# Kernel optimization log

Hardware: AMD Instinct MI355X
Metric: run time of the kernel (lower is better)

## Reference

```python
import jax, jax.numpy as jnp
import numpy as np

N_HEAD = 16

def _proj(W, b, x):
    # 1x1 Conv2d: x is (b, e, h, w) -> (b, o, h, w)
    return jnp.einsum('oe,behw->bohw', W, x) + b[None, :, None, None]

def setup_inputs() -> dict:
    key = jax.random.key(0)
    ks = jax.random.split(key, 12)
    B, E, S = 2, 1024, 2048
    d_qk, d_v, d_out = E, E, E
    def xavier(k, o, i):
        bound = np.sqrt(6.0 / (o + i))
        return jax.random.uniform(k, (o, i), jnp.float32, -bound, bound)
    return {
        'q': jax.random.normal(ks[0], (B, E, 1, S), jnp.float32),
        'k': jax.random.normal(ks[1], (B, E, 1, S), jnp.float32),
        'v': jax.random.normal(ks[2], (B, E, 1, S), jnp.float32),
        'qk_mask': jax.random.normal(ks[3], (B, S, 1, S), jnp.float32),
        'Wq': xavier(ks[4], d_qk, E), 'bq': jnp.zeros((d_qk,), jnp.float32),
        'Wk': xavier(ks[5], d_qk, E), 'bk': jnp.zeros((d_qk,), jnp.float32),
        'Wv': xavier(ks[6], d_v, E), 'bv': jnp.zeros((d_v,), jnp.float32),
        'Wo': xavier(ks[7], d_out, d_v), 'bo': jnp.zeros((d_out,), jnp.float32),
    }

def reference(q, k, v, qk_mask, Wq, bq, Wk, bk, Wv, bv, Wo, bo):
    # q,k,v: (B, E, 1, S); qk_mask: (B, S_src, 1, S_tgt)
    qp = _proj(Wq, bq, q)
    kp = _proj(Wk, bk, k)
    vp = _proj(Wv, bv, v)
    B, C, _, S = qp.shape
    H = N_HEAD
    dh = C // H
    scale = float(dh) ** -0.5
    qh = (qp * scale).reshape(B, H, dh, S)   # (b, h, c, q)
    kh = kp.reshape(B, H, dh, S)             # (b, h, c, k)
    vh = vp.reshape(B, H, dh, S)             # (b, h, c, k)
    # per-head scores, equivalent to the split einsum 'bchq,bkhc->bkhq'
    scores = jnp.einsum('bhcq,bhck->bhkq', qh, kh)        # (b, h, k, q)
    scores = scores + qk_mask[:, None, :, 0, :]           # mask broadcast over heads
    w = jax.nn.softmax(scores, axis=2)                    # softmax over key dim (dim=1 per-head)
    attn = jnp.einsum('bhkq,bhck->bhcq', w, vh).reshape(B, C, 1, S)
    return _proj(Wo, bo, attn)
```

## Files before the change

### kernel.cpp

```cpp
#include <hip/hip_runtime.h>
#include <hip/hip_bf16.h>

typedef unsigned short ushort_t;
typedef __attribute__((ext_vector_type(8))) __bf16 bf16x8;
typedef __attribute__((ext_vector_type(4))) float f32x4;
typedef __attribute__((ext_vector_type(2))) unsigned int u32x2;
typedef __attribute__((ext_vector_type(8))) unsigned short us8;

#define DEV __device__ __forceinline__

constexpr int BB = 2, EE = 1024, SS = 2048, HH = 16;
constexpr float L2E = 1.44269504088896f;
constexpr float SCALE_Q = 0.125f * 1.44269504088896f;

DEV ushort_t f2bf(float x) {
  union { float f; unsigned u; } c; c.f = x;
  unsigned u = c.u;
  return (ushort_t)((u + 0x7fffu + ((u >> 16) & 1u)) >> 16);
}

DEV unsigned cvtpk(float lo, float hi) {
  unsigned r;
  asm volatile("v_cvt_pk_bf16_f32 %0, %1, %2" : "=v"(r) : "v"(lo), "v"(hi));
  return r;
}

DEV void gload16(const void* g, void* l) {
  __builtin_amdgcn_global_load_lds((const __attribute__((address_space(1))) void*)g,
                                   (__attribute__((address_space(3))) void*)l, 16, 0, 0);
}

struct TpArgs { const float* i0; const float* i1; const float* i2;
                ushort_t* o0; ushort_t* o1; ushort_t* o2; };

__global__ __launch_bounds__(256) void k_transpose_cvt(TpArgs a) {
  int z = blockIdx.z; int p = z >> 1; int b = z & 1;
  const float* in = (p == 0) ? a.i0 : (p == 1) ? a.i1 : a.i2;
  ushort_t* out = (p == 0) ? a.o0 : (p == 1) ? a.o1 : a.o2;
  in += (long long)b * EE * SS;
  out += (long long)b * SS * EE;
  int s0 = blockIdx.x * 64, e0 = blockIdx.y * 64;
  __shared__ __align__(16) ushort_t T[64][72];
  int t = threadIdx.x;
  int sc = (t & 15) * 4, erb = t >> 4;
#pragma unroll
  for (int it = 0; it < 4; ++it) {
    int er = erb + it * 16;
    float4 v = *(const float4*)(in + (long long)(e0 + er) * SS + s0 + sc);
    T[sc + 0][er] = f2bf(v.x);
    T[sc + 1][er] = f2bf(v.y);
    T[sc + 2][er] = f2bf(v.z);
    T[sc + 3][er] = f2bf(v.w);
  }
  __syncthreads();
#pragma unroll
  for (int it = 0; it < 2; ++it) {
    int slot = t + it * 256;
    int sr = slot >> 3, ec = (slot & 7) * 8;
    us8 v = *(const us8*)&T[sr][ec];
    *(us8*)(out + (long long)(s0 + sr) * EE + e0 + ec) = v;
  }
}

struct WArgs { const float* w0; const float* w1; const float* w2; const float* w3;
               ushort_t* o0; ushort_t* o1; ushort_t* o2; ushort_t* o3; };

__global__ __launch_bounds__(256) void k_cvt_w(WArgs a) {
  int y = blockIdx.y;
  const float* in = (y == 0) ? a.w0 : (y == 1) ? a.w1 : (y == 2) ? a.w2 : a.w3;
  ushort_t* out = (y == 0) ? a.o0 : (y == 1) ? a.o1 : (y == 2) ? a.o2 : a.o3;
  long long idx = ((long long)blockIdx.x * 256 + threadIdx.x) * 4;
  float4 v = *(const float4*)(in + idx);
  unsigned lo = f2bf(v.x) | ((unsigned)f2bf(v.y) << 16);
  unsigned hi = f2bf(v.z) | ((unsigned)f2bf(v.w) << 16);
  u32x2 pk = {lo, hi};
  *(u32x2*)(out + idx) = pk;
}

DEV void stage_tile(const ushort_t* src0, ushort_t* dst0, int w, int lane) {
#pragma unroll
  for (int i = 0; i < 2; ++i) {
    int u = w * 128 + i * 64 + lane;
    int row = u >> 2, part = u & 3;
    gload16(src0 + (long long)row * 1024 + part * 8, dst0 + (w * 128 + i * 64) * 8);
  }
}

__global__ __launch_bounds__(256) void k_proj(
    const ushort_t* __restrict__ xq, const ushort_t* __restrict__ xk,
    const ushort_t* __restrict__ xv, const ushort_t* __restrict__ wq,
    const ushort_t* __restrict__ wk, const ushort_t* __restrict__ wv,
    const float* __restrict__ bqp, const float* __restrict__ bkp,
    const float* __restrict__ bvp,
    ushort_t* __restrict__ qpT, ushort_t* __restrict__ kpT,
    ushort_t* __restrict__ vpN) {
  constexpr int K = 1024;
  __shared__ __align__(16) ushort_t As[2][4096];
  __shared__ __align__(16) ushort_t Bs[2][4096];
  int t = threadIdx.x, lane = t & 63, w = t >> 6;
  int lq = lane & 15, g = lane >> 4;
  int z = blockIdx.z, pair = z >> 1, b = z & 1;
  long long s2 = (long long)SS * EE;
  int m0, n0, LDo; bool browq; float scale; const float* bias;
  const ushort_t *Ab, *Bb; ushort_t* Co;
  if (pair < 2) {
    m0 = blockIdx.y * 128; n0 = blockIdx.x * 128;
    Ab = (pair == 0 ? wq : wk) + (long long)m0 * K;
    Bb = (pair == 0 ? xq : xk) + b * s2 + (long long)n0 * K;
    Co = (pair == 0 ? qpT : kpT) + b * s2;
    bias = (pair == 0 ? bqp : bkp);
    scale = (pair == 0 ? SCALE_Q : 1.0f);
    LDo = EE; browq = true;
  } else {
    m0 = blockIdx.x * 128; n0 = blockIdx.y * 128;
    Ab = xv + b * s2 + (long long)m0 * K;
    Bb = wv + (long long)n0 * K;
    Co = vpN + b * s2;
    bias = bvp; scale = 1.0f; LDo = SS; browq = false;
  }

  f32x4 acc[4][4];
#pragma unroll
  for (int mi = 0; mi < 4; ++mi)
#pragma unroll
    for (int ni = 0; ni < 4; ++ni) acc[mi][ni] = (f32x4){0.f, 0.f, 0.f, 0.f};

  stage_tile(Ab, As[0], w, lane);
  stage_tile(Bb, Bs[0], w, lane);
  __syncthreads();
  int wm = w >> 1, wn = w & 1;
  for (int kt = 0; kt < K / 32; ++kt) {
    int buf = kt & 1;
    if (kt + 1 < K / 32) {
      stage_tile(Ab + (kt + 1) * 32, As[buf ^ 1], w, lane);
      stage_tile(Bb + (kt + 1) * 32, Bs[buf ^ 1], w, lane);
    }
    bf16x8 aF[4], bF[4];
#pragma unroll
    for (int mi = 0; mi < 4; ++mi)
      aF[mi] = *(const bf16x8*)&As[buf][(wm * 64 + mi * 16 + lq) * 32 + g * 8];
#pragma unroll
    for (int ni = 0; ni < 4; ++ni)
      bF[ni] = *(const bf16x8*)&Bs[buf][(wn * 64 + ni * 16 + lq) * 32 + g * 8];
#pragma unroll
    for (int mi = 0; mi < 4; ++mi)
#pragma unroll
      for (int ni = 0; ni < 4; ++ni)
        acc[mi][ni] = __builtin_amdgcn_mfma_f32_16x16x32_bf16(aF[mi], bF[ni], acc[mi][ni], 0, 0, 0);
    __syncthreads();
  }
#pragma unroll
  for (int ni = 0; ni < 4; ++ni) {
    int col = n0 + wn * 64 + ni * 16 + lq;
    float bc = browq ? 0.f : bias[col];
#pragma unroll
    for (int mi = 0; mi < 4; ++mi) {
      int row0 = m0 + wm * 64 + mi * 16 + 4 * g;
      f32x4 v = acc[mi][ni];
#pragma unroll
      for (int r = 0; r < 4; ++r) {
        float bb = browq ? bias[row0 + r] : bc;
        v[r] = (v[r] + bb) * scale;
      }
      u32x2 pk = {cvtpk(v[0], v[1]), cvtpk(v[2], v[3])};
      *(u32x2*)(Co + (long long)col * LDo + row0) = pk;
    }
  }
}

__global__ __launch_bounds__(256) void k_gemm_out(
    const ushort_t* __restrict__ A, long long sA,
    const ushort_t* __restrict__ Bm,
    float* __restrict__ C, long long sC,
    const float* __restrict__ bias, int LDo) {
  constexpr int K = 1024;
  __shared__ __align__(16) ushort_t As[2][4096];
  __shared__ __align__(16) ushort_t Bs[2][4096];
  int t = threadIdx.x, lane = t & 63, w = t >> 6;
  int lq = lane & 15, g = lane >> 4;
  int m0 = blockIdx.y * 128, n0 = blockIdx.x * 128;
  const ushort_t* Ab = A + (long long)blockIdx.z * sA + (long long)m0 * K;
  const ushort_t* Bb = Bm + (long long)n0 * K;

  f32x4 acc[4][4];
#pragma unroll
  for (int mi = 0; mi < 4; ++mi)
#pragma unroll
    for (int ni = 0; ni < 4; ++ni) acc[mi][ni] = (f32x4){0.f, 0.f, 0.f, 0.f};

  stage_tile(Ab, As[0], w, lane);
  stage_tile(Bb, Bs[0], w, lane);
  __syncthreads();
  int wm = w >> 1, wn = w & 1;
  for (int kt = 0; kt < K / 32; ++kt) {
    int buf = kt & 1;
    if (kt + 1 < K / 32) {
      stage_tile(Ab + (kt + 1) * 32, As[buf ^ 1], w, lane);
      stage_tile(Bb + (kt + 1) * 32, Bs[buf ^ 1], w, lane);
    }
    bf16x8 aF[4], bF[4];
#pragma unroll
    for (int mi = 0; mi < 4; ++mi)
      aF[mi] = *(const bf16x8*)&As[buf][(wm * 64 + mi * 16 + lq) * 32 + g * 8];
#pragma unroll
    for (int ni = 0; ni < 4; ++ni)
      bF[ni] = *(const bf16x8*)&Bs[buf][(wn * 64 + ni * 16 + lq) * 32 + g * 8];
#pragma unroll
    for (int mi = 0; mi < 4; ++mi)
#pragma unroll
      for (int ni = 0; ni < 4; ++ni)
        acc[mi][ni] = __builtin_amdgcn_mfma_f32_16x16x32_bf16(aF[mi], bF[ni], acc[mi][ni], 0, 0, 0);
    __syncthreads();
  }
#pragma unroll
  for (int ni = 0; ni < 4; ++ni) {
    int col = n0 + wn * 64 + ni * 16 + lq;
    float bc = bias[col];
#pragma unroll
    for (int mi = 0; mi < 4; ++mi) {
      int row0 = m0 + wm * 64 + mi * 16 + 4 * g;
      f32x4 v = acc[mi][ni];
#pragma unroll
      for (int r = 0; r < 4; ++r) v[r] += bc;
      *(f32x4*)(C + (long long)blockIdx.z * sC + (long long)col * LDo + row0) = v;
    }
  }
}

__global__ __launch_bounds__(256, 4) void k_attn(
    const ushort_t* __restrict__ qpT, const ushort_t* __restrict__ kpT,
    const ushort_t* __restrict__ vp, const float* __restrict__ mask,
    ushort_t* __restrict__ attnT) {
  int t = threadIdx.x, lane = t & 63, w = t >> 6;
  int lq = lane & 15, g = lane >> 4;
  int ksw = lq & 7;
  int vsw = (lq >> 1) & 3;
  int qt = blockIdx.x, h = blockIdx.y, b = blockIdx.z;
  int q0 = qt * 64;
  long long s2 = (long long)SS * EE;
  const ushort_t* qT = qpT + b * s2;
  const ushort_t* kTb = kpT + b * s2 + h * 64;
  const ushort_t* vB = vp + b * s2 + (long long)(h * 64) * SS;
  const float* mk = mask + (long long)b * SS * SS;
  ushort_t* aT = attnT + b * s2;

  __shared__ __align__(16) ushort_t Kt[2][2048];
  __shared__ __align__(16) ushort_t Vt[2][2048];
  __shared__ __align__(16) ushort_t Pt[4][512];

  int qglob = q0 + w * 16;
  const float* mbase = mk + qglob + lq;

  bf16x8 qF[2];
#pragma unroll
  for (int ch = 0; ch < 2; ++ch)
    qF[ch] = *(const bf16x8*)(qT + (long long)(qglob + lq) * EE + h * 64 + ch * 32 + g * 8);

  int krow = w * 8 + (lane >> 3), kslot = lane & 7;
  int vrow = w * 16 + (lane >> 2), vslot = lane & 3;
  auto stageKV = [&](int buf, int k0) {
    gload16(kTb + (long long)(k0 + krow) * EE + (kslot ^ (krow & 7)) * 8,
            &Kt[buf][w * 512]);
    gload16(vB + (long long)vrow * SS + k0 + (vslot ^ ((vrow >> 1) & 3)) * 8,
            &Vt[buf][w * 512]);
  };

  stageKV(0, 0);
  __syncthreads();

  f32x4 accO[4];
#pragma unroll
  for (int cf = 0; cf < 4; ++cf) accO[cf] = (f32x4){0.f, 0.f, 0.f, 0.f};
  float mrun = -3e38f, lrun = 0.f;

#pragma unroll 1
  for (int kt = 0; kt < SS / 32; ++kt) {
    int k0 = kt * 32;
    int cur = kt & 1;
    if (kt + 1 < SS / 32) stageKV(cur ^ 1, k0 + 32);

    float mv[2][4];
#pragma unroll
    for (int kf = 0; kf < 2; ++kf)
#pragma unroll
      for (int r = 0; r < 4; ++r)
        mv[kf][r] = mbase[(long long)(k0 + kf * 16 + 4 * g + r) * SS];

    f32x4 accS[2];
#pragma unroll
    for (int kf = 0; kf < 2; ++kf) accS[kf] = (f32x4){0.f, 0.f, 0.f, 0.f};
    __builtin_amdgcn_s_setprio(1);
#pragma unroll
    for (int ch = 0; ch < 2; ++ch) {
      bf16x8 aK[2];
#pragma unroll
      for (int kf = 0; kf < 2; ++kf) {
        int row = kf * 16 + lq;
        aK[kf] = *(const bf16x8*)&Kt[cur][row * 64 + (((ch * 4 + g) ^ ksw) * 8)];
      }
#pragma unroll
      for (int kf = 0; kf < 2; ++kf)
        accS[kf] = __builtin_amdgcn_mfma_f32_16x16x32_bf16(aK[kf], qF[ch], accS[kf], 0, 0, 0);
    }
    __builtin_amdgcn_s_setprio(0);

    float sv[2][4];
    float tm = -3e38f;
#pragma unroll
    for (int kf = 0; kf < 2; ++kf)
#pragma unroll
      for (int r = 0; r < 4; ++r) {
        sv[kf][r] = fmaf(mv[kf][r], L2E, accS[kf][r]);
        tm = fmaxf(tm, sv[kf][r]);
      }
    tm = fmaxf(tm, __shfl_xor(tm, 16));
    tm = fmaxf(tm, __shfl_xor(tm, 32));
    if (__any(tm > mrun + 8.0f)) {
      float mnew = fmaxf(mrun, tm);
      float corr = __builtin_amdgcn_exp2f(mrun - mnew);
      lrun *= corr;
#pragma unroll
      for (int cf = 0; cf < 4; ++cf) accO[cf] = accO[cf] * corr;
      mrun = mnew;
    }
    float ps = 0.f;
    unsigned pk0[2], pk1[2];
#pragma unroll
    for (int kf = 0; kf < 2; ++kf) {
      float p0 = __builtin_amdgcn_exp2f(sv[kf][0] - mrun);
      float p1 = __builtin_amdgcn_exp2f(sv[kf][1] - mrun);
      float p2 = __builtin_amdgcn_exp2f(sv[kf][2] - mrun);
      float p3 = __builtin_amdgcn_exp2f(sv[kf][3] - mrun);
      ps += (p0 + p1) + (p2 + p3);
      pk0[kf] = cvtpk(p0, p1);
      pk1[kf] = cvtpk(p2, p3);
    }
    ps += __shfl_xor(ps, 16);
    ps += __shfl_xor(ps, 32);
    lrun += ps;
#pragma unroll
    for (int kf = 0; kf < 2; ++kf) {
      int slot = (kf * 2 + (g >> 1)) ^ vsw;
      u32x2 pkv = {pk0[kf], pk1[kf]};
      *(u32x2*)&Pt[w][lq * 32 + slot * 8 + (g & 1) * 4] = pkv;
    }

    __builtin_amdgcn_s_setprio(1);
    bf16x8 bP = *(const bf16x8*)&Pt[w][lq * 32 + ((g ^ vsw) * 8)];
#pragma unroll
    for (int cf = 0; cf < 4; ++cf) {
      int row = cf * 16 + lq;
      bf16x8 vF = *(const bf16x8*)&Vt[cur][row * 32 + ((g ^ vsw) * 8)];
      accO[cf] = __builtin_amdgcn_mfma_f32_16x16x32_bf16(vF, bP, accO[cf], 0, 0, 0);
    }
    __builtin_amdgcn_s_setprio(0);
    __syncthreads();
  }

  float inv = 1.f / lrun;
  int s = qglob + lq;
#pragma unroll
  for (int cf = 0; cf < 4; ++cf) {
    int c0 = h * 64 + cf * 16 + 4 * g;
    f32x4 v = accO[cf];
    u32x2 pk = {cvtpk(v[0] * inv, v[1] * inv), cvtpk(v[2] * inv, v[3] * inv)};
    *(u32x2*)(aT + (long long)s * EE + c0) = pk;
  }
}

extern "C" void kernel_launch(void* const* d_in, const int* in_sizes, int n_in,
                              void* d_out, int out_size, void* d_ws, size_t ws_size,
                              hipStream_t stream) {
  const float* q = (const float*)d_in[0];
  const float* k = (const float*)d_in[1];
  const float* v = (const float*)d_in[2];
  const float* mask = (const float*)d_in[3];
  const float* Wq = (const float*)d_in[4];
  const float* bq = (const float*)d_in[5];
  const float* Wk = (const float*)d_in[6];
  const float* bk = (const float*)d_in[7];
  const float* Wv = (const float*)d_in[8];
  const float* bv = (const float*)d_in[9];
  const float* Wo = (const float*)d_in[10];
  const float* bo = (const float*)d_in[11];
  float* out = (float*)d_out;

  char* ws = (char*)d_ws;
  const long long MB = 1024LL * 1024LL;
  ushort_t* xqT = (ushort_t*)(ws + 0 * MB);
  ushort_t* xkT = (ushort_t*)(ws + 8 * MB);
  ushort_t* xvT = (ushort_t*)(ws + 16 * MB);
  ushort_t* wqB = (ushort_t*)(ws + 24 * MB);
  ushort_t* wkB = (ushort_t*)(ws + 26 * MB);
  ushort_t* wvB = (ushort_t*)(ws + 28 * MB);
  ushort_t* woB = (ushort_t*)(ws + 30 * MB);
  ushort_t* qpT = (ushort_t*)(ws + 32 * MB);
  ushort_t* kpT = (ushort_t*)(ws + 40 * MB);
  ushort_t* vpN = (ushort_t*)(ws + 48 * MB);
  ushort_t* anT = (ushort_t*)(ws + 56 * MB);

  TpArgs tp{q, k, v, xqT, xkT, xvT};
  hipLaunchKernelGGL(k_transpose_cvt, dim3(SS / 64, EE / 64, 6), dim3(256), 0, stream, tp);
  WArgs wa{Wq, Wk, Wv, Wo, wqB, wkB, wvB, woB};
  hipLaunchKernelGGL(k_cvt_w, dim3(1024, 4, 1), dim3(256), 0, stream, wa);

  hipLaunchKernelGGL(k_proj, dim3(SS / 128, EE / 128, 6), dim3(256), 0, stream,
                     xqT, xkT, xvT, wqB, wkB, wvB, bq, bk, bv, qpT, kpT, vpN);
  hipLaunchKernelGGL(k_attn, dim3(SS / 64, HH, BB), dim3(256), 0, stream,
                     qpT, kpT, vpN, mask, anT);
  long long s2 = (long long)SS * EE;
  hipLaunchKernelGGL(k_gemm_out, dim3(EE / 128, SS / 128, BB), dim3(256), 0, stream,
                     anT, s2, woB, out, s2, bo, SS);
}
```

Before: 172.0 us.

## Split attention key range in two and merge partial softmax results

The attention kernel now processes half of the key sequence per block, which doubles the grid. Each block writes unnormalized fp32 partial outputs plus its running max and sum. A new combine kernel merges the two halves with log-sum-exp weighting and writes the bf16 attention output. This adds parallelism and shorter per-block loops, but costs extra fp32 global traffic (about 32MB written and read), an extra launch, and workspace that overlaps the dead input-transpose buffers. The launch bounds occupancy hint was also dropped.

```diff
diff --git a/kernel.cpp b/kernel.cpp
--- a/kernel.cpp
+++ b/kernel.cpp
@@ -227,22 +227,23 @@
   }
 }
 
-__global__ __launch_bounds__(256, 4) void k_attn(
+__global__ __launch_bounds__(256) void k_attn(
     const ushort_t* __restrict__ qpT, const ushort_t* __restrict__ kpT,
     const ushort_t* __restrict__ vp, const float* __restrict__ mask,
-    ushort_t* __restrict__ attnT) {
+    float* __restrict__ Op, float* __restrict__ ml) {
   int t = threadIdx.x, lane = t & 63, w = t >> 6;
   int lq = lane & 15, g = lane >> 4;
   int ksw = lq & 7;
   int vsw = (lq >> 1) & 3;
-  int qt = blockIdx.x, h = blockIdx.y, b = blockIdx.z;
+  int qt = blockIdx.x, h = blockIdx.y, z = blockIdx.z;
+  int b = z & 1, sp = z >> 1;
   int q0 = qt * 64;
+  int ksta = sp * (SS / 2);
   long long s2 = (long long)SS * EE;
   const ushort_t* qT = qpT + b * s2;
   const ushort_t* kTb = kpT + b * s2 + h * 64;
   const ushort_t* vB = vp + b * s2 + (long long)(h * 64) * SS;
   const float* mk = mask + (long long)b * SS * SS;
-  ushort_t* aT = attnT + b * s2;
 
   __shared__ __align__(16) ushort_t Kt[2][2048];
   __shared__ __align__(16) ushort_t Vt[2][2048];
@@ -265,7 +266,7 @@
             &Vt[buf][w * 512]);
   };
 
-  stageKV(0, 0);
+  stageKV(0, ksta);
   __syncthreads();
 
   f32x4 accO[4];
@@ -274,10 +275,10 @@
   float mrun = -3e38f, lrun = 0.f;
 
 #pragma unroll 1
-  for (int kt = 0; kt < SS / 32; ++kt) {
-    int k0 = kt * 32;
+  for (int kt = 0; kt < SS / 2 / 32; ++kt) {
+    int k0 = ksta + kt * 32;
     int cur = kt & 1;
-    if (kt + 1 < SS / 32) stageKV(cur ^ 1, k0 + 32);
+    if (kt + 1 < SS / 2 / 32) stageKV(cur ^ 1, k0 + 32);
 
     float mv[2][4];
 #pragma unroll
@@ -357,15 +358,41 @@
     __syncthreads();
   }
 
-  float inv = 1.f / lrun;
   int s = qglob + lq;
+  long long obase = ((long long)(sp * 2 + b) * SS + s) * EE;
 #pragma unroll
   for (int cf = 0; cf < 4; ++cf) {
     int c0 = h * 64 + cf * 16 + 4 * g;
-    f32x4 v = accO[cf];
-    u32x2 pk = {cvtpk(v[0] * inv, v[1] * inv), cvtpk(v[2] * inv, v[3] * inv)};
-    *(u32x2*)(aT + (long long)s * EE + c0) = pk;
-  }
+    *(f32x4*)(Op + obase + c0) = accO[cf];
+  }
+  if (g == 0) {
+    float2 v2 = {mrun, lrun};
+    *(float2*)(ml + (((long long)(sp * 2 + b) * HH + h) * SS + s) * 2) = v2;
+  }
+}
+
+__global__ __launch_bounds__(256) void k_combine(
+    const float* __restrict__ Op, const float* __restrict__ ml,
+    ushort_t* __restrict__ anT) {
+  long long idx = (long long)blockIdx.x * 256 + threadIdx.x;
+  long long e = idx * 4;
+  int c = (int)(e & 1023);
+  int s = (int)((e >> 10) & 2047);
+  int b = (int)(e >> 21);
+  int h = c >> 6;
+  const float2* mlp = (const float2*)ml;
+  float2 ml0 = mlp[((long long)b * HH + h) * SS + s];
+  float2 ml1 = mlp[((long long)(2 + b) * HH + h) * SS + s];
+  float M = fmaxf(ml0.x, ml1.x);
+  float w0 = __builtin_amdgcn_exp2f(ml0.x - M);
+  float w1 = __builtin_amdgcn_exp2f(ml1.x - M);
+  float inv = 1.f / fmaf(ml0.y, w0, ml1.y * w1);
+  w0 *= inv; w1 *= inv;
+  f32x4 O0 = *(const f32x4*)(Op + ((long long)b * SS + s) * EE + c);
+  f32x4 O1 = *(const f32x4*)(Op + ((long long)(2 + b) * SS + s) * EE + c);
+  f32x4 o = O0 * w0 + O1 * w1;
+  u32x2 pk = {cvtpk(o[0], o[1]), cvtpk(o[2], o[3])};
+  *(u32x2*)(anT + (long long)b * SS * EE + (long long)s * EE + c) = pk;
 }
 
 extern "C" void kernel_launch(void* const* d_in, const int* in_sizes, int n_in,
@@ -387,17 +414,19 @@
 
   char* ws = (char*)d_ws;
   const long long MB = 1024LL * 1024LL;
+  float*    Opb = (float*)(ws + 0 * MB);
   ushort_t* xqT = (ushort_t*)(ws + 0 * MB);
   ushort_t* xkT = (ushort_t*)(ws + 8 * MB);
   ushort_t* xvT = (ushort_t*)(ws + 16 * MB);
   ushort_t* wqB = (ushort_t*)(ws + 24 * MB);
   ushort_t* wkB = (ushort_t*)(ws + 26 * MB);
   ushort_t* wvB = (ushort_t*)(ws + 28 * MB);
-  ushort_t* woB = (ushort_t*)(ws + 30 * MB);
-  ushort_t* qpT = (ushort_t*)(ws + 32 * MB);
-  ushort_t* kpT = (ushort_t*)(ws + 40 * MB);
-  ushort_t* vpN = (ushort_t*)(ws + 48 * MB);
-  ushort_t* anT = (ushort_t*)(ws + 56 * MB);
+  float*    mlb = (float*)(ws + 32 * MB);
+  ushort_t* woB = (ushort_t*)(ws + 33 * MB);
+  ushort_t* qpT = (ushort_t*)(ws + 35 * MB);
+  ushort_t* kpT = (ushort_t*)(ws + 43 * MB);
+  ushort_t* vpN = (ushort_t*)(ws + 51 * MB);
+  ushort_t* anT = (ushort_t*)(ws + 59 * MB);
 
   TpArgs tp{q, k, v, xqT, xkT, xvT};
   hipLaunchKernelGGL(k_transpose_cvt, dim3(SS / 64, EE / 64, 6), dim3(256), 0, stream, tp);
@@ -406,8 +435,9 @@
 
   hipLaunchKernelGGL(k_proj, dim3(SS / 128, EE / 128, 6), dim3(256), 0, stream,
                      xqT, xkT, xvT, wqB, wkB, wvB, bq, bk, bv, qpT, kpT, vpN);
-  hipLaunchKernelGGL(k_attn, dim3(SS / 64, HH, BB), dim3(256), 0, stream,
-                     qpT, kpT, vpN, mask, anT);
+  hipLaunchKernelGGL(k_attn, dim3(SS / 64, HH, BB * 2), dim3(256), 0, stream,
+                     qpT, kpT, vpN, mask, Opb, mlb);
+  hipLaunchKernelGGL(k_combine, dim3(4096), dim3(256), 0, stream, Opb, mlb, anT);
   long long s2 = (long long)SS * EE;
   hipLaunchKernelGGL(k_gemm_out, dim3(EE / 128, SS / 128, BB), dim3(256), 0, stream,
                      anT, s2, woB, out, s2, bo, SS);
```

Measured after the change: 191.7 us. 1.11x slower.
